# Kernel optimization log

Hardware: AMD Instinct MI355X
Metric: run time of the kernel (lower is better)

## Reference

```python
import jax, jax.numpy as jnp
import numpy as np

N_BLADES = 32  # Cl(4,1) has 2^5 = 32 basis blades


def _gp_sign_bitwise(a, b):
    """Sign of e_a * e_b in Cl(4,1) via bitwise swap counting (numpy, static)."""
    a = np.asarray(a, dtype=np.int64)
    b = np.asarray(b, dtype=np.int64)
    a, b = np.broadcast_arrays(a, b)
    swaps = np.zeros(a.shape, dtype=np.int64)
    for i in range(5):
        b_has_i = (b >> i) & 1
        mask_gt = (~((1 << (i + 1)) - 1)) & 31
        val = a & mask_gt
        pc = (val & 1) + ((val >> 1) & 1) + ((val >> 2) & 1) + ((val >> 3) & 1) + ((val >> 4) & 1)
        swaps += b_has_i * pc
    comm_sign = np.where(swaps % 2 == 0, 1.0, -1.0)
    metric_sign = np.where(((a & 16) & (b & 16)) > 0, -1.0, 1.0)
    return (comm_sign * metric_sign).astype(np.float32)


_M = np.arange(N_BLADES)
PERM = (_M[:, None] ^ _M[None, :]).astype(np.int32)        # PERM[k, m] = m ^ k
SIGNS = _gp_sign_bitwise(_M[None, :], PERM)                 # sign(m, m^k), [32, 32]
PERM_J = jnp.asarray(PERM)
SIGNS_J = jnp.asarray(SIGNS)


def setup_inputs() -> dict:
    key = jax.random.key(0)
    kx, kw = jax.random.split(key)
    B, In, Out = 1024, 256, 256
    x = jax.random.normal(kx, (B, In, N_BLADES), dtype=jnp.float32)
    std = 0.5 / (In * N_BLADES) ** 0.5
    weight = jax.random.normal(kw, (Out, In, N_BLADES), dtype=jnp.float32) * std
    return {"x": x, "weight": weight}


def reference(x, weight):
    # x: [B, In, 32], weight: [Out, In, 32]
    # out[b, o, k] = sum_{i, m} x[b, i, m^k] * sign(m, m^k) * w[o, i, m]
    x_g = x[..., PERM_J] * SIGNS_J                 # [B, In, 32(k), 32(m)]
    out = jnp.einsum('bikm,oim->bok', x_g, weight)  # [B, Out, 32]
    return out
```

## Files before the change

### kernel.cpp

```cpp
#include <hip/hip_runtime.h>

typedef __attribute__((ext_vector_type(8))) short bf16x8;
typedef __attribute__((ext_vector_type(16))) float f32x16;
typedef __attribute__((ext_vector_type(8))) unsigned short ushort8;

#define N_BLADES 32
#define B_DIM 1024
#define IN_DIM 256
#define OUT_DIM 256
#define K_DIM (IN_DIM * N_BLADES)
#define N_DIM (OUT_DIM * N_BLADES)


__device__ __forceinline__ unsigned short f2bf(float f) {
    unsigned int u = __float_as_uint(f);
    u = (u + 0x7fff + ((u >> 16) & 1)) >> 16;
    return (unsigned short)u;
}

__device__ __forceinline__ float gp_sign(int a, int b) {
    int swaps = 0;
#pragma unroll
    for (int i = 0; i < 5; ++i) {
        int mask = (~((1 << (i + 1)) - 1)) & 31;
        swaps += ((b >> i) & 1) * __popc(a & mask);
    }
    float s = (swaps & 1) ? -1.0f : 1.0f;
    if (a & b & 16) s = -s;
    return s;
}

__device__ __forceinline__ void gload_lds16(const void* g, void* l) {
    __builtin_amdgcn_global_load_lds(
        (const __attribute__((address_space(1))) unsigned int*)g,
        (__attribute__((address_space(3))) unsigned int*)l, 16, 0, 0);
}

#define FENCE() asm volatile("" ::: "memory")
#define BAR()    { FENCE(); __builtin_amdgcn_s_barrier(); FENCE(); }
#define SCHED0() __builtin_amdgcn_sched_barrier(0)
#define LGKM(n)  { asm volatile("s_waitcnt lgkmcnt(" #n ")" ::: "memory"); }
#define VMC(n)   { asm volatile("s_waitcnt vmcnt(" #n ")" ::: "memory"); }

__global__ __launch_bounds__(256) void cast_kernel(const float4* __restrict__ x,
                                                   unsigned short* __restrict__ xb) {
    int t = blockIdx.x * 256 + threadIdx.x;
    float4 a = x[t * 2];
    float4 b = x[t * 2 + 1];
    ushort8 pk;
    pk[0] = f2bf(a.x); pk[1] = f2bf(a.y); pk[2] = f2bf(a.z); pk[3] = f2bf(a.w);
    pk[4] = f2bf(b.x); pk[5] = f2bf(b.y); pk[6] = f2bf(b.z); pk[7] = f2bf(b.w);
    *(ushort8*)(xb + (size_t)t * 8) = pk;
}

__global__ __launch_bounds__(256) void cast_w_perm_kernel(const float* __restrict__ w,
                                                          unsigned short* __restrict__ wb2) {
    int t = blockIdx.x * 256 + threadIdx.x;
    int o31   = t & 31;
    int c16   = (t >> 5) & 7;
    int panel = (t >> 8) & 7;
    int kt    = t >> 11;
    int o  = panel * 32 + o31;
    int k0 = kt * 64 + c16 * 8;
    const float4* src = (const float4*)(w + (long)o * K_DIM + k0);
    float4 a = src[0], b = src[1];
    ushort8 pk;
    pk[0] = f2bf(a.x); pk[1] = f2bf(a.y); pk[2] = f2bf(a.z); pk[3] = f2bf(a.w);
    pk[4] = f2bf(b.x); pk[5] = f2bf(b.y); pk[6] = f2bf(b.z); pk[7] = f2bf(b.w);
    *(ushort8*)(wb2 + (size_t)t * 8) = pk;
}

__device__ __forceinline__ bf16x8 shuffle_sign(bf16x8 v, int jx,
                                               unsigned int m0, unsigned int m1,
                                               unsigned int m2, unsigned int m3) {
    union { bf16x8 v8; unsigned int w[4]; } a, b;
    a.v8 = v;
    int s = jx >> 1;
    unsigned int t0 = (s & 1) ? a.w[1] : a.w[0];
    unsigned int t1 = (s & 1) ? a.w[0] : a.w[1];
    unsigned int t2 = (s & 1) ? a.w[3] : a.w[2];
    unsigned int t3 = (s & 1) ? a.w[2] : a.w[3];
    unsigned int u0 = (s & 2) ? t2 : t0;
    unsigned int u1 = (s & 2) ? t3 : t1;
    unsigned int u2 = (s & 2) ? t0 : t2;
    unsigned int u3 = (s & 2) ? t1 : t3;
    if (jx & 1) {
        u0 = (u0 >> 16) | (u0 << 16);
        u1 = (u1 >> 16) | (u1 << 16);
        u2 = (u2 >> 16) | (u2 << 16);
        u3 = (u3 >> 16) | (u3 << 16);
    }
    b.w[0] = u0 ^ m0; b.w[1] = u1 ^ m1; b.w[2] = u2 ^ m2; b.w[3] = u3 ^ m3;
    return b.v8;
}


#define ROWB 16384

__global__ __launch_bounds__(512, 1) void gemm_ko32_kernel(const unsigned short* __restrict__ xb,
                                                           const unsigned short* __restrict__ wb2,
                                                           float* __restrict__ Cws) {
    __shared__ char lds[163840];

    const int tid  = threadIdx.x;
    const int lane = tid & 63;
    const int wid  = tid >> 6;
    const int wr   = wid >> 2;
    const int wc   = wid & 3;
    const int l31  = lane & 31;
    const int l5   = lane >> 5;

    const int  kblk = blockIdx.x;
    const long row0 = (long)blockIdx.y * 128;
    const int  jx   = kblk & 7;
    const int  kq   = (kblk >> 3) & 3;

    const int rA = tid >> 2;
    const int c0 = tid & 3;
    const char* aSrcK = (const char*)xb + (row0 + rA) * ROWB;
    const int aoffB = (c0 ^ kq) * 16;
    const int adst0 = (rA >> 5) * 4096 + c0 * 512 + (((rA & 31) ^ (c0 << 1)) * 16);

    unsigned int mk0, mk1, mk2, mk3;
    {
        unsigned int mw[4];
#pragma unroll
        for (int w_ = 0; w_ < 4; ++w_) {
            unsigned int m_ = 0;
#pragma unroll
            for (int e2 = 0; e2 < 2; ++e2) {
                int m = 8 * c0 + 2 * w_ + e2;
                if (gp_sign(m, m ^ kblk) < 0.0f) m_ |= 0x8000u << (16 * e2);
            }
            mw[w_] = m_;
        }
        mk0 = mw[0]; mk1 = mw[1]; mk2 = mw[2]; mk3 = mw[3];
    }

    const int  tid16 = tid * 16;
    const char* bSrc = (const char*)wb2 + tid16;

    const int aLp = wr * 8192;
    const int bLp = 32768 + wc * 8192;
    const int aC0 = (0 + l5) * 512 + ((l31 ^ (((0 + l5) & 3) << 1)) * 16);
    const int aC1 = (2 + l5) * 512 + ((l31 ^ (((2 + l5) & 3) << 1)) * 16);
    const int aC2 = (4 + l5) * 512 + ((l31 ^ (((4 + l5) & 3) << 1)) * 16);
    const int aC3 = (6 + l5) * 512 + ((l31 ^ (((6 + l5) & 3) << 1)) * 16);
    const int bC0 = (0 + l5) * 512 + l31 * 16;
    const int bC1 = (2 + l5) * 512 + l31 * 16;
    const int bC2 = (4 + l5) * 512 + l31 * 16;
    const int bC3 = (6 + l5) * 512 + l31 * 16;

#define B_STAGE(br, tb) { \
    _Pragma("unroll") for (int n = 0; n < 4; ++n) \
        gload_lds16(bSrc + (tb) + n * 8192, \
                    lds + 32768 + (br) * 32768 + n * 8192 + tid16); }
#define A_LOAD_E(kpb) { \
    rAe0 = *(const bf16x8*)(aSrcK + (kpb) + aoffB); \
    rAe1 = *(const bf16x8*)(aSrcK + (kpb) + aoffB + 64); }
#define A_LOAD_O(kpb) { \
    rAo0 = *(const bf16x8*)(aSrcK + (kpb) + aoffB); \
    rAo1 = *(const bf16x8*)(aSrcK + (kpb) + aoffB + 64); }
#define A_WRITE_E(ab) { \
    bf16x8 s0_ = shuffle_sign(rAe0, jx, mk0, mk1, mk2, mk3); \
    bf16x8 s1_ = shuffle_sign(rAe1, jx, mk0, mk1, mk2, mk3); \
    *(bf16x8*)(lds + (ab) * 16384 + adst0) = s0_; \
    *(bf16x8*)(lds + (ab) * 16384 + adst0 + 2048) = s1_; }
#define A_WRITE_O(ab) { \
    bf16x8 s0_ = shuffle_sign(rAo0, jx, mk0, mk1, mk2, mk3); \
    bf16x8 s1_ = shuffle_sign(rAo1, jx, mk0, mk1, mk2, mk3); \
    *(bf16x8*)(lds + (ab) * 16384 + adst0) = s0_; \
    *(bf16x8*)(lds + (ab) * 16384 + adst0 + 2048) = s1_; }

#define READ_G0(ab, br) { \
    aG0[0][0] = *(const bf16x8*)(lds + (ab)*16384 + aLp + 0*4096 + aC0); \
    aG0[0][1] = *(const bf16x8*)(lds + (ab)*16384 + aLp + 0*4096 + aC1); \
    aG0[1][0] = *(const bf16x8*)(lds + (ab)*16384 + aLp + 1*4096 + aC0); \
    aG0[1][1] = *(const bf16x8*)(lds + (ab)*16384 + aLp + 1*4096 + aC1); \
    bG0[0][0] = *(const bf16x8*)(lds + (br)*32768 + bLp + 0*4096 + bC0); \
    bG0[0][1] = *(const bf16x8*)(lds + (br)*32768 + bLp + 0*4096 + bC1); \
    bG0[1][0] = *(const bf16x8*)(lds + (br)*32768 + bLp + 1*4096 + bC0); \
    bG0[1][1] = *(const bf16x8*)(lds + (br)*32768 + bLp + 1*4096 + bC1); }
#define READ_G1(ab, br) { \
    aG1[0][0] = *(const bf16x8*)(lds + (ab)*16384 + aLp + 0*4096 + aC2); \
    aG1[0][1] = *(const bf16x8*)(lds + (ab)*16384 + aLp + 0*4096 + aC3); \
    aG1[1][0] = *(const bf16x8*)(lds + (ab)*16384 + aLp + 1*4096 + aC2); \
    aG1[1][1] = *(const bf16x8*)(lds + (ab)*16384 + aLp + 1*4096 + aC3); \
    bG1[0][0] = *(const bf16x8*)(lds + (br)*32768 + bLp + 0*4096 + bC2); \
    bG1[0][1] = *(const bf16x8*)(lds + (br)*32768 + bLp + 0*4096 + bC3); \
    bG1[1][0] = *(const bf16x8*)(lds + (br)*32768 + bLp + 1*4096 + bC2); \
    bG1[1][1] = *(const bf16x8*)(lds + (br)*32768 + bLp + 1*4096 + bC3); }
#define MFG0() \
    _Pragma("unroll") for (int s = 0; s < 2; ++s) \
    _Pragma("unroll") for (int mt = 0; mt < 2; ++mt) \
    _Pragma("unroll") for (int nt = 0; nt < 2; ++nt) \
        acc[mt][nt] = __builtin_amdgcn_mfma_f32_32x32x16_bf16(aG0[mt][s], bG0[nt][s], acc[mt][nt], 0, 0, 0);
#define MFG1() \
    _Pragma("unroll") for (int s = 0; s < 2; ++s) \
    _Pragma("unroll") for (int mt = 0; mt < 2; ++mt) \
    _Pragma("unroll") for (int nt = 0; nt < 2; ++nt) \
        acc[mt][nt] = __builtin_amdgcn_mfma_f32_32x32x16_bf16(aG1[mt][s], bG1[nt][s], acc[mt][nt], 0, 0, 0);

    f32x16 acc[2][2];
#pragma unroll
    for (int mt = 0; mt < 2; ++mt)
#pragma unroll
        for (int nt = 0; nt < 2; ++nt) acc[mt][nt] = (f32x16)0.0f;

    bf16x8 rAe0, rAe1, rAo0, rAo1;
    bf16x8 aG0[2][2], bG0[2][2], aG1[2][2], bG1[2][2];

    A_LOAD_E(0);
    SCHED0();
    B_STAGE(0, 0);
    SCHED0();
    VMC(4);
    A_WRITE_E(0);
    SCHED0();
    B_STAGE(1, 32768);
    SCHED0();
    A_LOAD_O(128);
    SCHED0();
    B_STAGE(2, 65536);
    SCHED0();
    VMC(10);
    LGKM(0);
    BAR();

#define TILE32(AB, ABN, BR, BRS, ALOAD, AWRITE, Texp) { \
    const int T_ = (Texp); \
    const int  kAr = ((T_ + 2) & 127) << 7; \
    const long kBg = (long)((T_ + 3) & 127) << 15; \
    VMC(4);                 \
    AWRITE(ABN); \
    SCHED0(); \
    READ_G0(AB, BR); \
    SCHED0(); \
    READ_G1(AB, BR); \
    SCHED0(); \
    ALOAD(kAr);             \
    SCHED0(); \
    B_STAGE(BRS, kBg);      \
    SCHED0(); \
    LGKM(8); MFG0(); \
    LGKM(0); MFG1(); \
    BAR(); }

    for (int t = 0; t < 32; ++t) {
        const int T4 = t * 4;
        TILE32(0, 1, 0, 3, A_LOAD_E, A_WRITE_O, T4);
        TILE32(1, 0, 1, 0, A_LOAD_O, A_WRITE_E, T4 + 1);
        TILE32(0, 1, 2, 1, A_LOAD_E, A_WRITE_O, T4 + 2);
        TILE32(1, 0, 3, 2, A_LOAD_O, A_WRITE_E, T4 + 3);
    }

#pragma unroll
    for (int mt = 0; mt < 2; ++mt)
#pragma unroll
        for (int nt = 0; nt < 2; ++nt) {
            long c = (long)kblk * 256 + wc * 64 + nt * 32 + l31;
#pragma unroll
            for (int r = 0; r < 16; ++r) {
                int  rl = (r & 3) + 8 * (r >> 2) + 4 * l5;
                long rb = row0 + wr * 64 + mt * 32 + rl;
                Cws[rb * N_DIM + c] = acc[mt][nt][r];
            }
        }

#undef B_STAGE
#undef A_LOAD_E
#undef A_LOAD_O
#undef A_WRITE_E
#undef A_WRITE_O
#undef READ_G0
#undef READ_G1
#undef MFG0
#undef MFG1
#undef TILE32
}

__global__ __launch_bounds__(256) void transpose_kernel(const float* __restrict__ Cws,
                                                        float* __restrict__ out) {
    __shared__ float t[32 * 260];
    const int tid = threadIdx.x;
    const long b  = blockIdx.x;
    const float4* src = (const float4*)(Cws + b * N_DIM);
    float4*       dst = (float4*)(out + b * N_DIM);
#pragma unroll
    for (int r = 0; r < 8; ++r) {
        int f = tid + r * 256;
        float4 v = src[f];
        int k  = f >> 6;
        int c4 = (f & 63) * 4;
        *(float4*)&t[k * 260 + c4] = v;
    }
    __syncthreads();
#pragma unroll
    for (int r = 0; r < 8; ++r) {
        int g  = tid + r * 256;
        int o  = g >> 3;
        int k0 = (g & 7) * 4;
        float4 v;
        v.x = t[(k0 + 0) * 260 + o];
        v.y = t[(k0 + 1) * 260 + o];
        v.z = t[(k0 + 2) * 260 + o];
        v.w = t[(k0 + 3) * 260 + o];
        dst[g] = v;
    }
}

__global__ __launch_bounds__(256) void fallback_gp_kernel(const float* __restrict__ x,
                                                          const float* __restrict__ w,
                                                          float* __restrict__ out) {
    __shared__ float xs[IN_DIM * 32];
    __shared__ float tab[1024];
    int tid = threadIdx.x;
    for (int idx = tid; idx < 1024; idx += 256) {
        int m = idx >> 5, k = idx & 31;
        tab[idx] = gp_sign(m, m ^ k);
    }
    int b = blockIdx.x;
    const float4* xrow = (const float4*)(x + (long)b * K_DIM);
    float4* xs4 = (float4*)xs;
    for (int idx = tid; idx < 2048; idx += 256) xs4[idx] = xrow[idx];
    __syncthreads();

    int wid = tid >> 6, lane = tid & 63;
    int o = blockIdx.y * 8 + wid;
    int k = lane & 31, half = lane >> 5;
    float acc = 0.f;
    const float* wrow = w + (long)o * K_DIM + half * 4096;
    for (int i = 0; i < 128; ++i) {
        int ib = (half * 128 + i) * 32;
#pragma unroll
        for (int m = 0; m < 32; ++m) {
            acc += xs[ib + (m ^ k)] * tab[m * 32 + k] * wrow[i * 32 + m];
        }
    }
    acc += __shfl_down(acc, 32);
    if (half == 0) out[((long)b * OUT_DIM + o) * 32 + k] = acc;
}

extern "C" void kernel_launch(void* const* d_in, const int* in_sizes, int n_in,
                              void* d_out, int out_size, void* d_ws, size_t ws_size,
                              hipStream_t stream) {
    const float* x = (const float*)d_in[0];
    const float* w = (const float*)d_in[1];
    float* out = (float*)d_out;

    const size_t xb_bytes  = (size_t)B_DIM * K_DIM * 2;
    const size_t wb_bytes  = (size_t)OUT_DIM * IN_DIM * 32 * 2;
    const size_t cw_bytes  = (size_t)B_DIM * N_DIM * 4;
    const size_t need = xb_bytes + wb_bytes + cw_bytes;

    if (ws_size >= need) {
        unsigned short* xbp = (unsigned short*)d_ws;
        unsigned short* wbp = (unsigned short*)((char*)d_ws + xb_bytes);
        float*          cws = (float*)((char*)d_ws + xb_bytes + wb_bytes);

        cast_kernel<<<dim3(4096), dim3(256), 0, stream>>>((const float4*)x, xbp);
        cast_w_perm_kernel<<<dim3(1024), dim3(256), 0, stream>>>(w, wbp);
        gemm_ko32_kernel<<<dim3(32, 8), dim3(512), 0, stream>>>(xbp, wbp, cws);
        transpose_kernel<<<dim3(B_DIM), dim3(256), 0, stream>>>(cws, out);
    } else {
        fallback_gp_kernel<<<dim3(B_DIM, OUT_DIM / 8), dim3(256), 0, stream>>>(x, w, out);
    }
}
```

Before: 162.2 us.

## Load A fragments directly from global into registers, bypassing LDS staging

Result: slower. 290.8 us (+79.3%).

```diff
diff --git a/kernel.cpp b/kernel.cpp
--- a/kernel.cpp
+++ b/kernel.cpp
@@ -42,15 +42,18 @@
 #define LGKM(n)  { asm volatile("s_waitcnt lgkmcnt(" #n ")" ::: "memory"); }
 #define VMC(n)   { asm volatile("s_waitcnt vmcnt(" #n ")" ::: "memory"); }
 
-__global__ __launch_bounds__(256) void cast_kernel(const float4* __restrict__ x,
-                                                   unsigned short* __restrict__ xb) {
+__global__ __launch_bounds__(256) void cast_x2_kernel(const float* __restrict__ x,
+                                                      unsigned short* __restrict__ xb2) {
     int t = blockIdx.x * 256 + threadIdx.x;
-    float4 a = x[t * 2];
-    float4 b = x[t * 2 + 1];
+    int o  = t & 7;
+    int b  = (t >> 3) & 1023;
+    int kt = t >> 13;
+    const float4* src = (const float4*)(x + (long)b * K_DIM + kt * 64 + o * 8);
+    float4 a = src[0], c = src[1];
     ushort8 pk;
     pk[0] = f2bf(a.x); pk[1] = f2bf(a.y); pk[2] = f2bf(a.z); pk[3] = f2bf(a.w);
-    pk[4] = f2bf(b.x); pk[5] = f2bf(b.y); pk[6] = f2bf(b.z); pk[7] = f2bf(b.w);
-    *(ushort8*)(xb + (size_t)t * 8) = pk;
+    pk[4] = f2bf(c.x); pk[5] = f2bf(c.y); pk[6] = f2bf(c.z); pk[7] = f2bf(c.w);
+    *(ushort8*)(xb2 + ((size_t)kt * 8192 + b * 8 + o) * 8) = pk;
 }
 
 __global__ __launch_bounds__(256) void cast_w_perm_kernel(const float* __restrict__ w,
@@ -95,12 +98,10 @@
 }
 
 
-#define ROWB 16384
-
-__global__ __launch_bounds__(512, 1) void gemm_ko32_kernel(const unsigned short* __restrict__ xb,
+__global__ __launch_bounds__(512, 1) void gemm_ko32_kernel(const unsigned short* __restrict__ xb2,
                                                            const unsigned short* __restrict__ wb2,
                                                            float* __restrict__ Cws) {
-    __shared__ char lds[163840];
+    __shared__ char lds[131072];
 
     const int tid  = threadIdx.x;
     const int lane = tid & 63;
@@ -115,37 +116,39 @@
     const int  jx   = kblk & 7;
     const int  kq   = (kblk >> 3) & 3;
 
-    const int rA = tid >> 2;
-    const int c0 = tid & 3;
-    const char* aSrcK = (const char*)xb + (row0 + rA) * ROWB;
-    const int aoffB = (c0 ^ kq) * 16;
-    const int adst0 = (rA >> 5) * 4096 + c0 * 512 + (((rA & 31) ^ (c0 << 1)) * 16);
-
-    unsigned int mk0, mk1, mk2, mk3;
+    const char* aX = (const char*)xb2;
+    const long rOff0 = (row0 + wr * 64 + l31) * 128;
+    const long rOff1 = rOff0 + 32 * 128;
+    const int o0 = (((0 * 2 + l5) ^ kq) & 7) * 16;
+    const int o1 = (((1 * 2 + l5) ^ kq) & 7) * 16;
+    const int o2 = (((2 * 2 + l5) ^ kq) & 7) * 16;
+    const int o3 = (((3 * 2 + l5) ^ kq) & 7) * 16;
+
+    unsigned int M0, M1, M2, M3, N0, N1, N2, N3;
     {
-        unsigned int mw[4];
-#pragma unroll
-        for (int w_ = 0; w_ < 4; ++w_) {
-            unsigned int m_ = 0;
-#pragma unroll
-            for (int e2 = 0; e2 < 2; ++e2) {
-                int m = 8 * c0 + 2 * w_ + e2;
-                if (gp_sign(m, m ^ kblk) < 0.0f) m_ |= 0x8000u << (16 * e2);
+        unsigned int mw[2][4];
+#pragma unroll
+        for (int u = 0; u < 2; ++u) {
+            int q = l5 + u * 2;
+#pragma unroll
+            for (int w_ = 0; w_ < 4; ++w_) {
+                unsigned int m_ = 0;
+#pragma unroll
+                for (int e2 = 0; e2 < 2; ++e2) {
+                    int m = 8 * q + 2 * w_ + e2;
+                    if (gp_sign(m, m ^ kblk) < 0.0f) m_ |= 0x8000u << (16 * e2);
+                }
+                mw[u][w_] = m_;
             }
-            mw[w_] = m_;
         }
-        mk0 = mw[0]; mk1 = mw[1]; mk2 = mw[2]; mk3 = mw[3];
+        M0 = mw[0][0]; M1 = mw[0][1]; M2 = mw[0][2]; M3 = mw[0][3];
+        N0 = mw[1][0]; N1 = mw[1][1]; N2 = mw[1][2]; N3 = mw[1][3];
     }
 
     const int  tid16 = tid * 16;
     const char* bSrc = (const char*)wb2 + tid16;
 
-    const int aLp = wr * 8192;
-    const int bLp = 32768 + wc * 8192;
-    const int aC0 = (0 + l5) * 512 + ((l31 ^ (((0 + l5) & 3) << 1)) * 16);
-    const int aC1 = (2 + l5) * 512 + ((l31 ^ (((2 + l5) & 3) << 1)) * 16);
-    const int aC2 = (4 + l5) * 512 + ((l31 ^ (((4 + l5) & 3) << 1)) * 16);
-    const int aC3 = (6 + l5) * 512 + ((l31 ^ (((6 + l5) & 3) << 1)) * 16);
+    const int bLp = wc * 8192;
     const int bC0 = (0 + l5) * 512 + l31 * 16;
     const int bC1 = (2 + l5) * 512 + l31 * 16;
     const int bC2 = (4 + l5) * 512 + l31 * 16;
@@ -154,52 +157,48 @@
 #define B_STAGE(br, tb) { \
     _Pragma("unroll") for (int n = 0; n < 4; ++n) \
         gload_lds16(bSrc + (tb) + n * 8192, \
-                    lds + 32768 + (br) * 32768 + n * 8192 + tid16); }
-#define A_LOAD_E(kpb) { \
-    rAe0 = *(const bf16x8*)(aSrcK + (kpb) + aoffB); \
-    rAe1 = *(const bf16x8*)(aSrcK + (kpb) + aoffB + 64); }
-#define A_LOAD_O(kpb) { \
-    rAo0 = *(const bf16x8*)(aSrcK + (kpb) + aoffB); \
-    rAo1 = *(const bf16x8*)(aSrcK + (kpb) + aoffB + 64); }
-#define A_WRITE_E(ab) { \
-    bf16x8 s0_ = shuffle_sign(rAe0, jx, mk0, mk1, mk2, mk3); \
-    bf16x8 s1_ = shuffle_sign(rAe1, jx, mk0, mk1, mk2, mk3); \
-    *(bf16x8*)(lds + (ab) * 16384 + adst0) = s0_; \
-    *(bf16x8*)(lds + (ab) * 16384 + adst0 + 2048) = s1_; }
-#define A_WRITE_O(ab) { \
-    bf16x8 s0_ = shuffle_sign(rAo0, jx, mk0, mk1, mk2, mk3); \
-    bf16x8 s1_ = shuffle_sign(rAo1, jx, mk0, mk1, mk2, mk3); \
-    *(bf16x8*)(lds + (ab) * 16384 + adst0) = s0_; \
-    *(bf16x8*)(lds + (ab) * 16384 + adst0 + 2048) = s1_; }
-
-#define READ_G0(ab, br) { \
-    aG0[0][0] = *(const bf16x8*)(lds + (ab)*16384 + aLp + 0*4096 + aC0); \
-    aG0[0][1] = *(const bf16x8*)(lds + (ab)*16384 + aLp + 0*4096 + aC1); \
-    aG0[1][0] = *(const bf16x8*)(lds + (ab)*16384 + aLp + 1*4096 + aC0); \
-    aG0[1][1] = *(const bf16x8*)(lds + (ab)*16384 + aLp + 1*4096 + aC1); \
+                    lds + (br) * 32768 + n * 8192 + tid16); }
+#define A_LOAD(S, kt) { \
+    const char* ab_ = aX + (long)(kt) * 131072; \
+    S##00 = *(const bf16x8*)(ab_ + rOff0 + o0); \
+    S##01 = *(const bf16x8*)(ab_ + rOff0 + o1); \
+    S##02 = *(const bf16x8*)(ab_ + rOff0 + o2); \
+    S##03 = *(const bf16x8*)(ab_ + rOff0 + o3); \
+    S##10 = *(const bf16x8*)(ab_ + rOff1 + o0); \
+    S##11 = *(const bf16x8*)(ab_ + rOff1 + o1); \
+    S##12 = *(const bf16x8*)(ab_ + rOff1 + o2); \
+    S##13 = *(const bf16x8*)(ab_ + rOff1 + o3); }
+#define A_SHUF(S) { \
+    f00 = shuffle_sign(S##00, jx, M0, M1, M2, M3); \
+    f01 = shuffle_sign(S##01, jx, N0, N1, N2, N3); \
+    f02 = shuffle_sign(S##02, jx, M0, M1, M2, M3); \
+    f03 = shuffle_sign(S##03, jx, N0, N1, N2, N3); \
+    f10 = shuffle_sign(S##10, jx, M0, M1, M2, M3); \
+    f11 = shuffle_sign(S##11, jx, N0, N1, N2, N3); \
+    f12 = shuffle_sign(S##12, jx, M0, M1, M2, M3); \
+    f13 = shuffle_sign(S##13, jx, N0, N1, N2, N3); }
+#define READ_B0(br) { \
     bG0[0][0] = *(const bf16x8*)(lds + (br)*32768 + bLp + 0*4096 + bC0); \
     bG0[0][1] = *(const bf16x8*)(lds + (br)*32768 + bLp + 0*4096 + bC1); \
     bG0[1][0] = *(const bf16x8*)(lds + (br)*32768 + bLp + 1*4096 + bC0); \
     bG0[1][1] = *(const bf16x8*)(lds + (br)*32768 + bLp + 1*4096 + bC1); }
-#define READ_G1(ab, br) { \
-    aG1[0][0] = *(const bf16x8*)(lds + (ab)*16384 + aLp + 0*4096 + aC2); \
-    aG1[0][1] = *(const bf16x8*)(lds + (ab)*16384 + aLp + 0*4096 + aC3); \
-    aG1[1][0] = *(const bf16x8*)(lds + (ab)*16384 + aLp + 1*4096 + aC2); \
-    aG1[1][1] = *(const bf16x8*)(lds + (ab)*16384 + aLp + 1*4096 + aC3); \
+#define READ_B1(br) { \
     bG1[0][0] = *(const bf16x8*)(lds + (br)*32768 + bLp + 0*4096 + bC2); \
     bG1[0][1] = *(const bf16x8*)(lds + (br)*32768 + bLp + 0*4096 + bC3); \
     bG1[1][0] = *(const bf16x8*)(lds + (br)*32768 + bLp + 1*4096 + bC2); \
     bG1[1][1] = *(const bf16x8*)(lds + (br)*32768 + bLp + 1*4096 + bC3); }
-#define MFG0() \
-    _Pragma("unroll") for (int s = 0; s < 2; ++s) \
-    _Pragma("unroll") for (int mt = 0; mt < 2; ++mt) \
-    _Pragma("unroll") for (int nt = 0; nt < 2; ++nt) \
-        acc[mt][nt] = __builtin_amdgcn_mfma_f32_32x32x16_bf16(aG0[mt][s], bG0[nt][s], acc[mt][nt], 0, 0, 0);
-#define MFG1() \
-    _Pragma("unroll") for (int s = 0; s < 2; ++s) \
-    _Pragma("unroll") for (int mt = 0; mt < 2; ++mt) \
-    _Pragma("unroll") for (int nt = 0; nt < 2; ++nt) \
-        acc[mt][nt] = __builtin_amdgcn_mfma_f32_32x32x16_bf16(aG1[mt][s], bG1[nt][s], acc[mt][nt], 0, 0, 0);
+#define MFG0() { \
+    _Pragma("unroll") for (int nt = 0; nt < 2; ++nt) { \
+        acc[0][nt] = __builtin_amdgcn_mfma_f32_32x32x16_bf16(f00, bG0[nt][0], acc[0][nt], 0, 0, 0); \
+        acc[1][nt] = __builtin_amdgcn_mfma_f32_32x32x16_bf16(f10, bG0[nt][0], acc[1][nt], 0, 0, 0); \
+        acc[0][nt] = __builtin_amdgcn_mfma_f32_32x32x16_bf16(f01, bG0[nt][1], acc[0][nt], 0, 0, 0); \
+        acc[1][nt] = __builtin_amdgcn_mfma_f32_32x32x16_bf16(f11, bG0[nt][1], acc[1][nt], 0, 0, 0); } }
+#define MFG1() { \
+    _Pragma("unroll") for (int nt = 0; nt < 2; ++nt) { \
+        acc[0][nt] = __builtin_amdgcn_mfma_f32_32x32x16_bf16(f02, bG1[nt][0], acc[0][nt], 0, 0, 0); \
+        acc[1][nt] = __builtin_amdgcn_mfma_f32_32x32x16_bf16(f12, bG1[nt][0], acc[1][nt], 0, 0, 0); \
+        acc[0][nt] = __builtin_amdgcn_mfma_f32_32x32x16_bf16(f03, bG1[nt][1], acc[0][nt], 0, 0, 0); \
+        acc[1][nt] = __builtin_amdgcn_mfma_f32_32x32x16_bf16(f13, bG1[nt][1], acc[1][nt], 0, 0, 0); } }
 
     f32x16 acc[2][2];
 #pragma unroll
@@ -207,51 +206,44 @@
 #pragma unroll
         for (int nt = 0; nt < 2; ++nt) acc[mt][nt] = (f32x16)0.0f;
 
-    bf16x8 rAe0, rAe1, rAo0, rAo1;
-    bf16x8 aG0[2][2], bG0[2][2], aG1[2][2], bG1[2][2];
-
-    A_LOAD_E(0);
+    bf16x8 aE00, aE01, aE02, aE03, aE10, aE11, aE12, aE13;
+    bf16x8 aO00, aO01, aO02, aO03, aO10, aO11, aO12, aO13;
+    bf16x8 f00, f01, f02, f03, f10, f11, f12, f13;
+    bf16x8 bG0[2][2], bG1[2][2];
+
+    A_LOAD(aE, 0);
     SCHED0();
     B_STAGE(0, 0);
-    SCHED0();
-    VMC(4);
-    A_WRITE_E(0);
-    SCHED0();
     B_STAGE(1, 32768);
     SCHED0();
-    A_LOAD_O(128);
+    A_LOAD(aO, 1);
     SCHED0();
     B_STAGE(2, 65536);
     SCHED0();
-    VMC(10);
-    LGKM(0);
+    VMC(16);
     BAR();
 
-#define TILE32(AB, ABN, BR, BRS, ALOAD, AWRITE, Texp) { \
+#define TILE32(BR, BRS, S, Texp) { \
     const int T_ = (Texp); \
-    const int  kAr = ((T_ + 2) & 127) << 7; \
-    const long kBg = (long)((T_ + 3) & 127) << 15; \
+    READ_B0(BR); \
+    READ_B1(BR); \
     VMC(4);                 \
-    AWRITE(ABN); \
+    A_SHUF(S); \
     SCHED0(); \
-    READ_G0(AB, BR); \
+    A_LOAD(S, (T_ + 2) & 127);                   \
     SCHED0(); \
-    READ_G1(AB, BR); \
+    B_STAGE(BRS, (long)((T_ + 3) & 127) << 15);  \
     SCHED0(); \
-    ALOAD(kAr);             \
-    SCHED0(); \
-    B_STAGE(BRS, kBg);      \
-    SCHED0(); \
-    LGKM(8); MFG0(); \
+    LGKM(4); MFG0(); \
     LGKM(0); MFG1(); \
     BAR(); }
 
     for (int t = 0; t < 32; ++t) {
         const int T4 = t * 4;
-        TILE32(0, 1, 0, 3, A_LOAD_E, A_WRITE_O, T4);
-        TILE32(1, 0, 1, 0, A_LOAD_O, A_WRITE_E, T4 + 1);
-        TILE32(0, 1, 2, 1, A_LOAD_E, A_WRITE_O, T4 + 2);
-        TILE32(1, 0, 3, 2, A_LOAD_O, A_WRITE_E, T4 + 3);
+        TILE32(0, 3, aE, T4);
+        TILE32(1, 0, aO, T4 + 1);
+        TILE32(2, 1, aE, T4 + 2);
+        TILE32(3, 2, aO, T4 + 3);
     }
 
 #pragma unroll
@@ -268,12 +260,10 @@
         }
 
 #undef B_STAGE
-#undef A_LOAD_E
-#undef A_LOAD_O
-#undef A_WRITE_E
-#undef A_WRITE_O
-#undef READ_G0
-#undef READ_G1
+#undef A_LOAD
+#undef A_SHUF
+#undef READ_B0
+#undef READ_B1
 #undef MFG0
 #undef MFG1
 #undef TILE32
@@ -358,7 +348,7 @@
         unsigned short* wbp = (unsigned short*)((char*)d_ws + xb_bytes);
         float*          cws = (float*)((char*)d_ws + xb_bytes + wb_bytes);
 
-        cast_kernel<<<dim3(4096), dim3(256), 0, stream>>>((const float4*)x, xbp);
+        cast_x2_kernel<<<dim3(4096), dim3(256), 0, stream>>>(x, xbp);
         cast_w_perm_kernel<<<dim3(1024), dim3(256), 0, stream>>>(w, wbp);
         gemm_ko32_kernel<<<dim3(32, 8), dim3(512), 0, stream>>>(xbp, wbp, cws);
         transpose_kernel<<<dim3(B_DIM), dim3(256), 0, stream>>>(cws, out);
```
